# Kernel tuning notes

Hardware: AMD Instinct MI355X
Metric: run time of the kernel (lower is better)

## Reference

```python
import jax, jax.numpy as jnp
import numpy as np

N_NODES = 50000
N_EDGES = 800000
FEATURES = 64
HIDDEN = 128
OUT_DIM = 64
CUTOFF = 10.0
STEP = 0.1
N_MU = 100  # len(arange(0, 10, 0.1))


def setup_inputs() -> dict:
    key = jax.random.key(0)
    k_h, k_src, k_dst, k_norm, k_w1, k_w2 = jax.random.split(key, 6)
    h = jax.random.normal(k_h, (N_NODES, FEATURES), dtype=jnp.float32)
    src = jax.random.randint(k_src, (N_EDGES,), 0, N_NODES, dtype=jnp.int64)
    dst = jax.random.randint(k_dst, (N_EDGES,), 0, N_NODES, dtype=jnp.int64)
    edge_norm = jax.random.uniform(k_norm, (N_EDGES,), dtype=jnp.float32) * CUTOFF
    mu = jnp.arange(0.0, CUTOFF, STEP, dtype=jnp.float32)  # [100], learned param
    in_dim = 2 * FEATURES + N_MU
    # xavier_normal with gain split across 2 linear layers: layer_gain = 1.0
    s1 = float(np.sqrt(2.0 / (in_dim + HIDDEN)))
    s2 = float(np.sqrt(2.0 / (HIDDEN + OUT_DIM)))
    W1 = jax.random.normal(k_w1, (HIDDEN, in_dim), dtype=jnp.float32) * s1
    W2 = jax.random.normal(k_w2, (OUT_DIM, HIDDEN), dtype=jnp.float32) * s2
    return {"h": h, "src": src, "dst": dst, "edge_norm": edge_norm,
            "mu": mu, "W1": W1, "W2": W2}


def reference(h, src, dst, edge_norm, mu, W1, W2):
    # Gaussian RBF expansion of edge distances: [E, n_mu]
    d_emb = jnp.exp((-1.0 / STEP) * (mu[None, :] - edge_norm[:, None]) ** 2)
    # gather endpoint features and concat: [E, 2*features + n_mu]
    x = jnp.concatenate((h[src], h[dst], d_emb), axis=-1)
    # MLP: Linear(no bias) -> SiLU -> Linear(no bias)
    hdn = jax.nn.silu(x @ W1.T)
    return hdn @ W2.T
```

## Files before the change

kernel.cpp:

```cpp
#include <hip/hip_runtime.h>
#include <hip/hip_bf16.h>


#define FEAT      64
#define NMU       100
#define K1_REAL   228
#define WEDGES    32
#define NWAVES    8
#define BEDGES    (WEDGES * NWAVES)
#define HN8       400000
#define B1N_ELEMS 30720
#define B2N_ELEMS 8192
#define RBF_C     0.81873075f

typedef __bf16  bf16x8 __attribute__((ext_vector_type(8)));
typedef __bf16  bf16x2 __attribute__((ext_vector_type(2)));
typedef float   fx16   __attribute__((ext_vector_type(16)));

__global__ void pack_w(const float* __restrict__ W1, const float* __restrict__ W2,
                       __bf16* __restrict__ B1, __bf16* __restrict__ B2) {
    int i = blockIdx.x * 256 + threadIdx.x;
    if (i < B1N_ELEMS) {
        int j   = i & 7;
        int n   = (i >> 3) & 127;
        int ksh = i >> 10;
        int k   = ksh * 8 + j;
        float v = (k < K1_REAL) ? W1[n * K1_REAL + k] : 0.0f;
        B1[i] = (__bf16)v;
    } else if (i < B1N_ELEMS + B2N_ELEMS) {
        int t    = i - B1N_ELEMS;
        int j    = t & 7;
        int slot = (t >> 3) & 63;
        int sh   = t >> 9;
        int r    = slot & 31;
        int n2t  = slot >> 5;
        int f    = (((r >> 2) & 1) << 4) | ((r >> 3) << 2) | (r & 3);
        int rho  = ((sh >> 2) << 5) | (((sh >> 1) & 1) << 4)
                 | ((j >> 2) << 3) | ((sh & 1) << 2) | (j & 3);
        B2[t] = (__bf16)W2[(n2t * 32 + f) * 128 + rho];
    }
}

__global__ void pack_h(const float* __restrict__ h, __bf16* __restrict__ hb) {
    int i = blockIdx.x * 256 + threadIdx.x;
    if (i >= HN8) return;
    const float4* p = (const float4*)h + (size_t)i * 2;
    float4 v0 = p[0];
    float4 v1 = p[1];
    bf16x8 b = { (__bf16)v0.x, (__bf16)v0.y, (__bf16)v0.z, (__bf16)v0.w,
                 (__bf16)v1.x, (__bf16)v1.y, (__bf16)v1.z, (__bf16)v1.w };
    ((bf16x8*)hb)[i] = b;
}

__device__ __forceinline__ bf16x8 hfrag_f32(const float* __restrict__ h, int node, int cb) {
    const float4* p = (const float4*)(h + (size_t)node * FEAT + cb);
    float4 v0 = p[0];
    float4 v1 = p[1];
    bf16x8 a = { (__bf16)v0.x, (__bf16)v0.y, (__bf16)v0.z, (__bf16)v0.w,
                 (__bf16)v1.x, (__bf16)v1.y, (__bf16)v1.z, (__bf16)v1.w };
    return a;
}

__device__ __forceinline__ float silu(float z) {
    return z * __builtin_amdgcn_rcpf(1.0f + __expf(-z));
}

template<bool HB16>
__global__
__attribute__((amdgpu_flat_work_group_size(512, 512), amdgpu_waves_per_eu(4)))
void edges_fused(const float* __restrict__ h,
                 const __bf16* __restrict__ hb,
                 const int*   __restrict__ src,
                 const int*   __restrict__ dst,
                 const float* __restrict__ enorm,
                 const float* __restrict__ mu,
                 const __bf16* __restrict__ B1,
                 const __bf16* __restrict__ B2,
                 float* __restrict__ out,
                 int E) {
    __shared__ __align__(16) __bf16 B1s[B1N_ELEMS];
    __shared__ __align__(16) __bf16 B2s[B2N_ELEMS];

    const int tid = threadIdx.x;
    const int w   = tid >> 6;
    const int m   = tid & 31;
    const int h5  = (tid >> 5) & 1;
    const int g0  = blockIdx.x * BEDGES + w * WEDGES;
    const bool act = (g0 < E);

    int ndst;
    float dval;
    bf16x8 ags[4];
    if (act) {
        int e = g0 + m;
        int nsrc = src[e];
        ndst = dst[e];
        dval = enorm[e];
#pragma unroll
        for (int ks = 0; ks < 4; ++ks) {
            const int cb = ks * 16 + h5 * 8;
            if constexpr (HB16)
                ags[ks] = *(const bf16x8*)(hb + (size_t)nsrc * FEAT + cb);
            else
                ags[ks] = hfrag_f32(h, nsrc, cb);
        }
    }

    {
        const bf16x8* gB1 = (const bf16x8*)B1;
        const bf16x8* gB2 = (const bf16x8*)B2;
        bf16x8* sB1 = (bf16x8*)B1s;
        bf16x8* sB2 = (bf16x8*)B2s;
#pragma unroll
        for (int it = 0; it < 8; ++it) {
            int g = it * 512 + tid;
            if (g < B1N_ELEMS / 8) sB1[g] = gB1[g];
        }
#pragma unroll
        for (int it = 0; it < 2; ++it) {
            int g = it * 512 + tid;
            sB2[g] = gB2[g];
        }
    }
    __syncthreads();
    if (!act) return;

    fx16 acc1[4] = {};

#pragma unroll
    for (int ks = 8; ks < 14; ++ks) {
        const int c0 = ks * 16 - 128 + h5 * 8;
        const float t0 = mu[c0] - dval;
        float v = __expf(-10.f * t0 * t0);
        float rr = __expf(-2.f * t0 - 0.1f);
        float e0 = v, e1, e2, e3, e4, e5, e6, e7;
        v *= rr; rr *= RBF_C; e1 = v;
        v *= rr; rr *= RBF_C; e2 = v;
        v *= rr; rr *= RBF_C; e3 = v;
        v *= rr; rr *= RBF_C; e4 = v;
        v *= rr; rr *= RBF_C; e5 = v;
        v *= rr; rr *= RBF_C; e6 = v;
        v *= rr;              e7 = v;
        bf16x8 a = { (__bf16)e0, (__bf16)e1, (__bf16)e2, (__bf16)e3,
                     (__bf16)e4, (__bf16)e5, (__bf16)e6, (__bf16)e7 };
        const int base = ((ks * 2 + h5) * 128 + m) * 8;
#pragma unroll
        for (int nt1 = 0; nt1 < 4; ++nt1) {
            bf16x8 a1 = *(const bf16x8*)&B1s[base + nt1 * 256];
            acc1[nt1] = __builtin_amdgcn_mfma_f32_32x32x16_bf16(a1, a, acc1[nt1], 0, 0, 0);
        }
    }
    {
        float4 m7 = *(const float4*)(mu + 96);
        const float d = dval;
        const bool lo = (h5 == 0);
        const __bf16 zz = (__bf16)0.0f;
        float t0 = m7.x - d, t1 = m7.y - d, t2 = m7.z - d, t3 = m7.w - d;
        bf16x8 a = { lo ? (__bf16)__expf(-10.f * t0 * t0) : zz,
                     lo ? (__bf16)__expf(-10.f * t1 * t1) : zz,
                     lo ? (__bf16)__expf(-10.f * t2 * t2) : zz,
                     lo ? (__bf16)__expf(-10.f * t3 * t3) : zz,
                     zz, zz, zz, zz };
        const int base = ((14 * 2 + h5) * 128 + m) * 8;
#pragma unroll
        for (int nt1 = 0; nt1 < 4; ++nt1) {
            bf16x8 a1 = *(const bf16x8*)&B1s[base + nt1 * 256];
            acc1[nt1] = __builtin_amdgcn_mfma_f32_32x32x16_bf16(a1, a, acc1[nt1], 0, 0, 0);
        }
    }
#pragma unroll
    for (int ks = 0; ks < 4; ++ks) {
        const int base = ((ks * 2 + h5) * 128 + m) * 8;
#pragma unroll
        for (int nt1 = 0; nt1 < 4; ++nt1) {
            bf16x8 a1 = *(const bf16x8*)&B1s[base + nt1 * 256];
            acc1[nt1] = __builtin_amdgcn_mfma_f32_32x32x16_bf16(a1, ags[ks], acc1[nt1], 0, 0, 0);
        }
    }
#pragma unroll
    for (int ks = 0; ks < 4; ++ks) {
        const int cb = ks * 16 + h5 * 8;
        if constexpr (HB16)
            ags[ks] = *(const bf16x8*)(hb + (size_t)ndst * FEAT + cb);
        else
            ags[ks] = hfrag_f32(h, ndst, cb);
    }
#pragma unroll
    for (int ks = 4; ks < 8; ++ks) {
        const int base = ((ks * 2 + h5) * 128 + m) * 8;
#pragma unroll
        for (int nt1 = 0; nt1 < 4; ++nt1) {
            bf16x8 a1 = *(const bf16x8*)&B1s[base + nt1 * 256];
            acc1[nt1] = __builtin_amdgcn_mfma_f32_32x32x16_bf16(a1, ags[ks - 4], acc1[nt1], 0, 0, 0);
        }
    }

    uint32_t P[32];
#pragma unroll
    for (int nt1 = 0; nt1 < 4; ++nt1) {
#pragma unroll
        for (int gp = 0; gp < 8; ++gp) {
            union { bf16x2 v; uint32_t u; } cv;
            cv.v = (bf16x2){ (__bf16)silu(acc1[nt1][2 * gp]),
                             (__bf16)silu(acc1[nt1][2 * gp + 1]) };
            P[nt1 * 8 + gp] = cv.u;
        }
    }

    fx16 acc2[2] = {};
#pragma unroll
    for (int s = 0; s < 8; ++s) {
        union { uint32_t u[4]; bf16x8 v; } uu;
        uu.u[0] = P[4 * s + 0]; uu.u[1] = P[4 * s + 1];
        uu.u[2] = P[4 * s + 2]; uu.u[3] = P[4 * s + 3];
        const int base2 = ((s * 2 + h5) * 64 + m) * 8;
#pragma unroll
        for (int n2t = 0; n2t < 2; ++n2t) {
            bf16x8 a2 = *(const bf16x8*)&B2s[base2 + n2t * 256];
            acc2[n2t] = __builtin_amdgcn_mfma_f32_32x32x16_bf16(a2, uu.v, acc2[n2t], 0, 0, 0);
        }
    }

    float* orow = out + (size_t)(g0 + m) * 64 + h5 * 16;
#pragma unroll
    for (int n2t = 0; n2t < 2; ++n2t)
#pragma unroll
        for (int qd = 0; qd < 4; ++qd) {
            float4 st = { acc2[n2t][4 * qd + 0], acc2[n2t][4 * qd + 1],
                          acc2[n2t][4 * qd + 2], acc2[n2t][4 * qd + 3] };
            *(float4*)(orow + n2t * 32 + qd * 4) = st;
        }
}

extern "C" void kernel_launch(void* const* d_in, const int* in_sizes, int n_in,
                              void* d_out, int out_size, void* d_ws, size_t ws_size,
                              hipStream_t stream) {
    const float* h   = (const float*)d_in[0];
    const int*   src = (const int*)d_in[1];
    const int*   dst = (const int*)d_in[2];
    const float* en  = (const float*)d_in[3];
    const float* mu  = (const float*)d_in[4];
    const float* W1  = (const float*)d_in[5];
    const float* W2  = (const float*)d_in[6];

    __bf16* B1 = (__bf16*)d_ws;
    __bf16* B2 = (__bf16*)((char*)d_ws + 61440);
    __bf16* HB = (__bf16*)((char*)d_ws + 77824);

    const size_t ws_needed = 77824 + (size_t)HN8 * 8 * sizeof(__bf16);
    const bool   use_hb    = ws_size >= ws_needed;

    pack_w<<<(B1N_ELEMS + B2N_ELEMS) / 256, 256, 0, stream>>>(W1, W2, B1, B2);

    const int E = in_sizes[1];
    const int nblocks = (E + BEDGES - 1) / BEDGES;

    if (use_hb) {
        pack_h<<<(HN8 + 255) / 256, 256, 0, stream>>>(h, HB);
        edges_fused<true><<<nblocks, 512, 0, stream>>>(h, HB, src, dst, en, mu, B1, B2, (float*)d_out, E);
    } else {
        edges_fused<false><<<nblocks, 512, 0, stream>>>(h, nullptr, src, dst, en, mu, B1, B2, (float*)d_out, E);
    }
}
```

Before: 298.4 us.

## Split layer-1 MFMA into two hidden-column passes and prefetch dst features early

Layer-1 accumulation is split into two passes, each covering two of the four 32-column hidden tiles, so only two fx16 accumulators are live at a time instead of four, with SiLU packing done per pass. The dst-node gathers are issued at kernel start alongside the src gathers, so their latency overlaps the weight staging into shared memory. The aim is lower register pressure (possibly higher occupancy) and earlier memory-level parallelism. The cost is recomputing the RBF exponentials twice, and the extra agd registers may offset the savings.

```diff
diff --git a/kernel.cpp b/kernel.cpp
--- a/kernel.cpp
+++ b/kernel.cpp
@@ -88,21 +88,24 @@
     const int g0  = blockIdx.x * BEDGES + w * WEDGES;
     const bool act = (g0 < E);
 
-    int ndst;
     float dval;
     bf16x8 ags[4];
+    bf16x8 agd[4];
     if (act) {
         int e = g0 + m;
         int nsrc = src[e];
-        ndst = dst[e];
+        int ndst = dst[e];
         dval = enorm[e];
 #pragma unroll
         for (int ks = 0; ks < 4; ++ks) {
             const int cb = ks * 16 + h5 * 8;
-            if constexpr (HB16)
+            if constexpr (HB16) {
                 ags[ks] = *(const bf16x8*)(hb + (size_t)nsrc * FEAT + cb);
-            else
+                agd[ks] = *(const bf16x8*)(hb + (size_t)ndst * FEAT + cb);
+            } else {
                 ags[ks] = hfrag_f32(h, nsrc, cb);
+                agd[ks] = hfrag_f32(h, ndst, cb);
+            }
         }
     }
 
@@ -125,86 +128,74 @@
     __syncthreads();
     if (!act) return;
 
-    fx16 acc1[4] = {};
-
-#pragma unroll
-    for (int ks = 8; ks < 14; ++ks) {
-        const int c0 = ks * 16 - 128 + h5 * 8;
-        const float t0 = mu[c0] - dval;
-        float v = __expf(-10.f * t0 * t0);
-        float rr = __expf(-2.f * t0 - 0.1f);
-        float e0 = v, e1, e2, e3, e4, e5, e6, e7;
-        v *= rr; rr *= RBF_C; e1 = v;
-        v *= rr; rr *= RBF_C; e2 = v;
-        v *= rr; rr *= RBF_C; e3 = v;
-        v *= rr; rr *= RBF_C; e4 = v;
-        v *= rr; rr *= RBF_C; e5 = v;
-        v *= rr; rr *= RBF_C; e6 = v;
-        v *= rr;              e7 = v;
-        bf16x8 a = { (__bf16)e0, (__bf16)e1, (__bf16)e2, (__bf16)e3,
-                     (__bf16)e4, (__bf16)e5, (__bf16)e6, (__bf16)e7 };
-        const int base = ((ks * 2 + h5) * 128 + m) * 8;
-#pragma unroll
-        for (int nt1 = 0; nt1 < 4; ++nt1) {
-            bf16x8 a1 = *(const bf16x8*)&B1s[base + nt1 * 256];
-            acc1[nt1] = __builtin_amdgcn_mfma_f32_32x32x16_bf16(a1, a, acc1[nt1], 0, 0, 0);
-        }
-    }
-    {
-        float4 m7 = *(const float4*)(mu + 96);
-        const float d = dval;
-        const bool lo = (h5 == 0);
-        const __bf16 zz = (__bf16)0.0f;
-        float t0 = m7.x - d, t1 = m7.y - d, t2 = m7.z - d, t3 = m7.w - d;
-        bf16x8 a = { lo ? (__bf16)__expf(-10.f * t0 * t0) : zz,
-                     lo ? (__bf16)__expf(-10.f * t1 * t1) : zz,
-                     lo ? (__bf16)__expf(-10.f * t2 * t2) : zz,
-                     lo ? (__bf16)__expf(-10.f * t3 * t3) : zz,
-                     zz, zz, zz, zz };
-        const int base = ((14 * 2 + h5) * 128 + m) * 8;
-#pragma unroll
-        for (int nt1 = 0; nt1 < 4; ++nt1) {
-            bf16x8 a1 = *(const bf16x8*)&B1s[base + nt1 * 256];
-            acc1[nt1] = __builtin_amdgcn_mfma_f32_32x32x16_bf16(a1, a, acc1[nt1], 0, 0, 0);
-        }
-    }
-#pragma unroll
-    for (int ks = 0; ks < 4; ++ks) {
-        const int base = ((ks * 2 + h5) * 128 + m) * 8;
-#pragma unroll
-        for (int nt1 = 0; nt1 < 4; ++nt1) {
-            bf16x8 a1 = *(const bf16x8*)&B1s[base + nt1 * 256];
-            acc1[nt1] = __builtin_amdgcn_mfma_f32_32x32x16_bf16(a1, ags[ks], acc1[nt1], 0, 0, 0);
-        }
-    }
-#pragma unroll
-    for (int ks = 0; ks < 4; ++ks) {
-        const int cb = ks * 16 + h5 * 8;
-        if constexpr (HB16)
-            ags[ks] = *(const bf16x8*)(hb + (size_t)ndst * FEAT + cb);
-        else
-            ags[ks] = hfrag_f32(h, ndst, cb);
-    }
-#pragma unroll
-    for (int ks = 4; ks < 8; ++ks) {
-        const int base = ((ks * 2 + h5) * 128 + m) * 8;
-#pragma unroll
-        for (int nt1 = 0; nt1 < 4; ++nt1) {
-            bf16x8 a1 = *(const bf16x8*)&B1s[base + nt1 * 256];
-            acc1[nt1] = __builtin_amdgcn_mfma_f32_32x32x16_bf16(a1, ags[ks - 4], acc1[nt1], 0, 0, 0);
-        }
-    }
-
     uint32_t P[32];
-#pragma unroll
-    for (int nt1 = 0; nt1 < 4; ++nt1) {
-#pragma unroll
-        for (int gp = 0; gp < 8; ++gp) {
-            union { bf16x2 v; uint32_t u; } cv;
-            cv.v = (bf16x2){ (__bf16)silu(acc1[nt1][2 * gp]),
-                             (__bf16)silu(acc1[nt1][2 * gp + 1]) };
-            P[nt1 * 8 + gp] = cv.u;
-        }
+
+#pragma unroll
+    for (int p = 0; p < 2; ++p) {
+        fx16 acc[2] = {};
+        const int tb0 = (2 * p) * 256;
+        const int tb1 = (2 * p + 1) * 256;
+
+#pragma unroll
+        for (int ks = 8; ks < 14; ++ks) {
+            const int c0 = ks * 16 - 128 + h5 * 8;
+            const float t0 = mu[c0] - dval;
+            float v = __expf(-10.f * t0 * t0);
+            float rr = __expf(-2.f * t0 - 0.1f);
+            float e0 = v, e1, e2, e3, e4, e5, e6, e7;
+            v *= rr; rr *= RBF_C; e1 = v;
+            v *= rr; rr *= RBF_C; e2 = v;
+            v *= rr; rr *= RBF_C; e3 = v;
+            v *= rr; rr *= RBF_C; e4 = v;
+            v *= rr; rr *= RBF_C; e5 = v;
+            v *= rr; rr *= RBF_C; e6 = v;
+            v *= rr;              e7 = v;
+            bf16x8 a = { (__bf16)e0, (__bf16)e1, (__bf16)e2, (__bf16)e3,
+                         (__bf16)e4, (__bf16)e5, (__bf16)e6, (__bf16)e7 };
+            const int base = ((ks * 2 + h5) * 128 + m) * 8;
+            bf16x8 a0 = *(const bf16x8*)&B1s[base + tb0];
+            bf16x8 a1 = *(const bf16x8*)&B1s[base + tb1];
+            acc[0] = __builtin_amdgcn_mfma_f32_32x32x16_bf16(a0, a, acc[0], 0, 0, 0);
+            acc[1] = __builtin_amdgcn_mfma_f32_32x32x16_bf16(a1, a, acc[1], 0, 0, 0);
+        }
+        {
+            float4 m7 = *(const float4*)(mu + 96);
+            const float d = dval;
+            const bool lo = (h5 == 0);
+            const __bf16 zz = (__bf16)0.0f;
+            float t0 = m7.x - d, t1 = m7.y - d, t2 = m7.z - d, t3 = m7.w - d;
+            bf16x8 a = { lo ? (__bf16)__expf(-10.f * t0 * t0) : zz,
+                         lo ? (__bf16)__expf(-10.f * t1 * t1) : zz,
+                         lo ? (__bf16)__expf(-10.f * t2 * t2) : zz,
+                         lo ? (__bf16)__expf(-10.f * t3 * t3) : zz,
+                         zz, zz, zz, zz };
+            const int base = ((14 * 2 + h5) * 128 + m) * 8;
+            bf16x8 a0 = *(const bf16x8*)&B1s[base + tb0];
+            bf16x8 a1 = *(const bf16x8*)&B1s[base + tb1];
+            acc[0] = __builtin_amdgcn_mfma_f32_32x32x16_bf16(a0, a, acc[0], 0, 0, 0);
+            acc[1] = __builtin_amdgcn_mfma_f32_32x32x16_bf16(a1, a, acc[1], 0, 0, 0);
+        }
+#pragma unroll
+        for (int ks = 0; ks < 8; ++ks) {
+            bf16x8 x = (ks < 4) ? ags[ks] : agd[ks - 4];
+            const int base = ((ks * 2 + h5) * 128 + m) * 8;
+            bf16x8 a0 = *(const bf16x8*)&B1s[base + tb0];
+            bf16x8 a1 = *(const bf16x8*)&B1s[base + tb1];
+            acc[0] = __builtin_amdgcn_mfma_f32_32x32x16_bf16(a0, x, acc[0], 0, 0, 0);
+            acc[1] = __builtin_amdgcn_mfma_f32_32x32x16_bf16(a1, x, acc[1], 0, 0, 0);
+        }
+
+#pragma unroll
+        for (int c = 0; c < 2; ++c)
+#pragma unroll
+            for (int gp = 0; gp < 8; ++gp) {
+                union { bf16x2 v; uint32_t u; } cv;
+                cv.v = (bf16x2){ (__bf16)silu(acc[c][2 * gp]),
+                                 (__bf16)silu(acc[c][2 * gp + 1]) };
+                P[(2 * p + c) * 8 + gp] = cv.u;
+            }
+
+        __builtin_amdgcn_sched_barrier(0);
     }
 
     fx16 acc2[2] = {};
```

Measured after the change: 302.7 us. Within noise of the previous version (+1.4%).
